# Optimization experiments

Measured on AMD Instinct MI355X. Metric: run time of the kernel, lower is better.

## Reference

```python
import jax, jax.numpy as jnp
import numpy as np

B, N, D = 2, 2048, 1024
H = 16
HS = D // H
EPS = 1e-6


def layer_norm(x, scale, bias):
    mu = jnp.mean(x, axis=-1, keepdims=True)
    var = jnp.mean(jnp.square(x - mu), axis=-1, keepdims=True)
    return (x - mu) * jax.lax.rsqrt(var + EPS) * scale + bias


def setup_inputs() -> dict:
    key = jax.random.key(0)
    ks = jax.random.split(key, 8)
    lecun = lambda k, shape: jax.random.normal(k, shape, jnp.float32) / jnp.sqrt(shape[0])
    return {
        "x": jax.random.normal(ks[0], (B, N, D), jnp.float32),
        "ln1_scale": jnp.ones((D,), jnp.float32),
        "ln1_bias": jnp.zeros((D,), jnp.float32),
        "w_qkv": lecun(ks[1], (D, 3 * D)),
        "w_out": lecun(ks[2], (D, D)),
        "b_out": jnp.zeros((D,), jnp.float32),
        "ln2_scale": jnp.ones((D,), jnp.float32),
        "ln2_bias": jnp.zeros((D,), jnp.float32),
        "w1": lecun(ks[3], (D, 2 * D)),
        "b1": jnp.zeros((2 * D,), jnp.float32),
        "w2": lecun(ks[4], (2 * D, D)),
        "b2": jnp.zeros((D,), jnp.float32),
    }


def reference(x, ln1_scale, ln1_bias, w_qkv, w_out, b_out,
              ln2_scale, ln2_bias, w1, b1, w2, b2):
    b, n, d = x.shape
    # --- attention sub-block ---
    xn = layer_norm(x, ln1_scale, ln1_bias)
    qkv = xn @ w_qkv                      # [B,N,3D]
    q, k, v = jnp.split(qkv, 3, axis=-1)
    q = q.reshape(b, n, H, HS)
    k = k.reshape(b, n, H, HS)
    v = v.reshape(b, n, H, HS)
    scores = jnp.einsum('bihd,bjhd->bhij', q, k) / jnp.sqrt(jnp.float32(HS))
    causal = jnp.tril(jnp.ones((n, n), bool))[None, None]
    scores = jnp.where(causal, scores, -jnp.inf)
    attn = jax.nn.softmax(scores, axis=-1)
    out_heads = jnp.einsum('bhij,bjhd->bihd', attn, v).reshape(b, n, d)
    x = x + out_heads @ w_out + b_out
    xn2 = layer_norm(x, ln2_scale, ln2_bias)
    y = jax.nn.gelu(xn2 @ w1 + b1)        # flax nn.gelu default approximate=True
    x = x + (y @ w2 + b2)
    return x
```

## Files before the change

### kernel.cpp

```cpp
#include <hip/hip_runtime.h>

#define D_MODEL 1024
#define NSEQ    2048
#define NBATCH  2
#define NHEAD   16
#define HSZ     64
#define MROWS   4096

typedef short s8v  __attribute__((ext_vector_type(8)));
typedef float f32x4 __attribute__((ext_vector_type(4)));

#define AS1(p) ((__attribute__((address_space(1))) const void*)(p))
#define AS3(p) ((__attribute__((address_space(3))) void*)(p))

__device__ __forceinline__ float b2f(unsigned short s) {
    union { unsigned u; float f; } z; z.u = (unsigned)s << 16; return z.f;
}
__device__ __forceinline__ unsigned short f2b(float f) {
    union { float f; unsigned u; } z; z.f = f;
    unsigned r = z.u + 0x7fffu + ((z.u >> 16) & 1u);
    return (unsigned short)(r >> 16);
}
__device__ __forceinline__ unsigned short f2b_trunc(float f) {
    union { float f; unsigned u; } z; z.f = f;
    return (unsigned short)(z.u >> 16);
}
__device__ __forceinline__ float gelu_f(float x) {
    float u = 0.7978845608028654f * (x + 0.044715f * x * x * x);
    float t = 1.f - 2.f / (1.f + __expf(2.f * u));
    return 0.5f * x * (1.f + t);
}

__global__ __launch_bounds__(256) void sniff_k(const unsigned short* __restrict__ xr,
                                               int* __restrict__ flag) {
    __shared__ int cnt[4];
    int tid = threadIdx.x, ok = 0;
    for (int i = tid; i < 2048; i += 256) {
        unsigned short u = xr[i];
        int e = (u >> 7) & 0xFF;
        if (u == 0 || (e >= 110 && e <= 135)) ok++;
    }
    #pragma unroll
    for (int off = 32; off; off >>= 1) ok += __shfl_down(ok, off);
    if ((tid & 63) == 0) cnt[tid >> 6] = ok;
    __syncthreads();
    if (tid == 0) {
        int tot = cnt[0] + cnt[1] + cnt[2] + cnt[3];
        *flag = (tot > 1843) ? 1 : 0;
    }
}

__global__ __launch_bounds__(256) void cvt_small_k(
    const void* p0, const void* p1, const void* p2, const void* p3,
    const void* p4, const void* p5, const void* p6,
    unsigned short* __restrict__ out, const int* __restrict__ flag)
{
    int i = blockIdx.x * 256 + threadIdx.x;
    const void* src; int off;
    if      (i < 1024) { src = p0; off = i; }
    else if (i < 2048) { src = p1; off = i - 1024; }
    else if (i < 3072) { src = p2; off = i - 2048; }
    else if (i < 4096) { src = p3; off = i - 3072; }
    else if (i < 5120) { src = p4; off = i - 4096; }
    else if (i < 7168) { src = p5; off = i - 5120; }
    else               { src = p6; off = i - 7168; }
    out[i] = (*flag) ? ((const unsigned short*)src)[off]
                     : f2b(((const float*)src)[off]);
}

__global__ __launch_bounds__(256) void transpose_all_k(
    const void* wqkv, const void* wout, const void* w1, const void* w2,
    unsigned short* t_qkv, unsigned short* t_out,
    unsigned short* t_w1, unsigned short* t_w2, const int* __restrict__ flag)
{
    __shared__ unsigned short t[32][33];
    int bid = blockIdx.x;
    const void* W; unsigned short* Wt; int K, N, bx, by;
    if      (bid < 3072) { W = wqkv; Wt = t_qkv; K = 1024; N = 3072; bx = bid % 96; by = bid / 96; }
    else if (bid < 4096) { bid -= 3072; W = wout; Wt = t_out; K = 1024; N = 1024; bx = bid % 32; by = bid / 32; }
    else if (bid < 6144) { bid -= 4096; W = w1;   Wt = t_w1;  K = 1024; N = 2048; bx = bid % 64; by = bid / 64; }
    else                 { bid -= 6144; W = w2;   Wt = t_w2;  K = 2048; N = 1024; bx = bid % 32; by = bid / 32; }
    int f = *flag;
    int n0 = bx * 32, k0 = by * 32;
    int x = threadIdx.x & 31, y = threadIdx.x >> 5;
    #pragma unroll
    for (int r = 0; r < 32; r += 8) {
        size_t idx = (size_t)(k0 + r + y) * N + n0 + x;
        t[r + y][x] = f ? ((const unsigned short*)W)[idx]
                        : f2b(((const float*)W)[idx]);
    }
    __syncthreads();
    #pragma unroll
    for (int r = 0; r < 32; r += 8)
        Wt[(size_t)(n0 + r + y) * K + k0 + x] = t[x][r + y];
}

__global__ __launch_bounds__(256) void ln1f_k(
    const void* __restrict__ x_raw, const unsigned short* __restrict__ scale,
    const unsigned short* __restrict__ bias, unsigned short* __restrict__ xb,
    unsigned short* __restrict__ xn, const int* __restrict__ flag)
{
    int row = blockIdx.x, tid = threadIdx.x;
    int f = *flag;
    float v[4], s = 0.f, s2 = 0.f;
    #pragma unroll
    for (int i = 0; i < 4; ++i) {
        size_t idx = (size_t)row * D_MODEL + tid + i * 256;
        float t = f ? b2f(((const unsigned short*)x_raw)[idx])
                    : ((const float*)x_raw)[idx];
        v[i] = t; s += t; s2 += t * t;
    }
    #pragma unroll
    for (int off = 32; off; off >>= 1) { s += __shfl_down(s, off); s2 += __shfl_down(s2, off); }
    __shared__ float rs[4], rs2[4];
    int w = tid >> 6;
    if ((tid & 63) == 0) { rs[w] = s; rs2[w] = s2; }
    __syncthreads();
    float S  = rs[0] + rs[1] + rs[2] + rs[3];
    float S2 = rs2[0] + rs2[1] + rs2[2] + rs2[3];
    float mean = S * (1.f / D_MODEL);
    float var  = S2 * (1.f / D_MODEL) - mean * mean;
    float rstd = rsqrtf(var + 1e-6f);
    #pragma unroll
    for (int i = 0; i < 4; ++i) {
        int d = tid + i * 256;
        size_t idx = (size_t)row * D_MODEL + d;
        xb[idx] = f2b(v[i]);
        xn[idx] = f2b((v[i] - mean) * rstd * b2f(scale[d]) + b2f(bias[d]));
    }
}

__global__ __launch_bounds__(256) void ln_k(
    const unsigned short* __restrict__ x, const unsigned short* __restrict__ scale,
    const unsigned short* __restrict__ bias, unsigned short* __restrict__ out)
{
    int row = blockIdx.x, tid = threadIdx.x;
    const unsigned short* xr = x + (size_t)row * D_MODEL;
    float v[4], s = 0.f, s2 = 0.f;
    #pragma unroll
    for (int i = 0; i < 4; ++i) {
        float t = b2f(xr[tid + i * 256]);
        v[i] = t; s += t; s2 += t * t;
    }
    #pragma unroll
    for (int off = 32; off; off >>= 1) { s += __shfl_down(s, off); s2 += __shfl_down(s2, off); }
    __shared__ float rs[4], rs2[4];
    int w = tid >> 6;
    if ((tid & 63) == 0) { rs[w] = s; rs2[w] = s2; }
    __syncthreads();
    float S  = rs[0] + rs[1] + rs[2] + rs[3];
    float S2 = rs2[0] + rs2[1] + rs2[2] + rs2[3];
    float mean = S * (1.f / D_MODEL);
    float var  = S2 * (1.f / D_MODEL) - mean * mean;
    float rstd = rsqrtf(var + 1e-6f);
    #pragma unroll
    for (int i = 0; i < 4; ++i) {
        int d = tid + i * 256;
        out[(size_t)row * D_MODEL + d] =
            f2b((v[i] - mean) * rstd * b2f(scale[d]) + b2f(bias[d]));
    }
}

template<int TN, int ACT, int RES, int ODYN>
__global__ __launch_bounds__(256) void gemm128_k(
    const unsigned short* __restrict__ A, const unsigned short* __restrict__ Bt,
    const unsigned short* __restrict__ bias, const unsigned short* __restrict__ resid,
    void* __restrict__ Cp, int M, int Nn, int K, const int* __restrict__ flag)
{
    constexpr int MT = (TN == 128) ? 4 : 2;
    __shared__ short As[128 * 64];
    __shared__ short Bs[TN * 64];
    int tid = threadIdx.x;
    int m0 = blockIdx.y * 128, n0 = blockIdx.x * TN;
    int lane = tid & 63, w = tid >> 6;
    int a_base = (TN == 128) ? (w >> 1) * 64 : w * 32;
    int b_base = (TN == 128) ? (w & 1) * 64 : 0;
    int mm = lane & 15, q = lane >> 4;

    f32x4 zero = {0.f, 0.f, 0.f, 0.f};
    f32x4 acc[MT][4];
    #pragma unroll
    for (int mt = 0; mt < MT; ++mt)
        #pragma unroll
        for (int nt = 0; nt < 4; ++nt) acc[mt][nt] = zero;

    int grow   = lane >> 3;
    int gchunk = ((lane & 7) ^ grow) * 8;
    const unsigned short* Ab = A  + (size_t)(m0 + w * 32 + grow) * K + gchunk;
    const unsigned short* Bb = Bt + (size_t)(n0 + w * (TN / 4) + grow) * K + gchunk;
    int swz = (mm & 7);

    for (int k0 = 0; k0 < K; k0 += 64) {
        __syncthreads();
        #pragma unroll
        for (int s = 0; s < 4; ++s)
            __builtin_amdgcn_global_load_lds(AS1(Ab + k0 + (size_t)(s * 8) * K),
                                             AS3(&As[(w * 32 + s * 8) * 64]), 16, 0, 0);
        #pragma unroll
        for (int s = 0; s < TN / 32; ++s)
            __builtin_amdgcn_global_load_lds(AS1(Bb + k0 + (size_t)(s * 8) * K),
                                             AS3(&Bs[(w * (TN / 4) + s * 8) * 64]), 16, 0, 0);
        __syncthreads();
        #pragma unroll
        for (int kk = 0; kk < 2; ++kk) {
            int col = ((kk * 4 + q) ^ swz) * 8;
            s8v af[MT], bf[4];
            #pragma unroll
            for (int mt = 0; mt < MT; ++mt)
                af[mt] = *(const s8v*)&As[(a_base + mt * 16 + mm) * 64 + col];
            #pragma unroll
            for (int nt = 0; nt < 4; ++nt)
                bf[nt] = *(const s8v*)&Bs[(b_base + nt * 16 + mm) * 64 + col];
            #pragma unroll
            for (int mt = 0; mt < MT; ++mt)
                #pragma unroll
                for (int nt = 0; nt < 4; ++nt)
                    acc[mt][nt] = __builtin_amdgcn_mfma_f32_16x16x32_bf16(
                        af[mt], bf[nt], acc[mt][nt], 0, 0, 0);
        }
    }

    int f = ODYN ? *flag : 1;
    #pragma unroll
    for (int nt = 0; nt < 4; ++nt) {
        int gc = n0 + b_base + nt * 16 + mm;
        float bv = bias ? b2f(bias[gc]) : 0.f;
        #pragma unroll
        for (int mt = 0; mt < MT; ++mt) {
            #pragma unroll
            for (int r = 0; r < 4; ++r) {
                int gr = m0 + a_base + mt * 16 + q * 4 + r;
                float v = acc[mt][nt][r] + bv;
                if (ACT == 1) v = gelu_f(v);
                if (RES == 1) v += b2f(resid[(size_t)gr * Nn + gc]);
                if (f) ((unsigned short*)Cp)[(size_t)gr * Nn + gc] = f2b(v);
                else   ((float*)Cp)[(size_t)gr * Nn + gc] = v;
            }
        }
    }
}

__global__ __launch_bounds__(256, 3) void fattn_k(
    const unsigned short* __restrict__ qkv, unsigned short* __restrict__ attn_out)
{
    int bh = blockIdx.x;
    int h = bh & (NHEAD - 1), b = bh >> 4;
    int qt = gridDim.y - 1 - blockIdx.y;
    int q0 = qt * 64;
    size_t base = (size_t)b * NSEQ * (3 * D_MODEL);

    __shared__ __align__(16) short Ks[128][72];
    __shared__ __align__(16) short Vts[64][136];
    __shared__ __align__(16) short Ps[64][136];

    int tid = threadIdx.x, lane = tid & 63, w = tid >> 6;
    int mm = lane & 15, q = lane >> 4;

    s8v qf[2];
    #pragma unroll
    for (int kk = 0; kk < 2; ++kk)
        qf[kk] = *(const s8v*)(qkv + base + (size_t)(q0 + w * 16 + mm) * (3 * D_MODEL)
                               + h * HSZ + kk * 32 + q * 8);

    f32x4 zero = {0.f, 0.f, 0.f, 0.f};
    f32x4 acc_o[4] = {zero, zero, zero, zero};
    float l_acc[4] = {0.f, 0.f, 0.f, 0.f};

    int kr = tid >> 1;
    int kc = (tid & 1) * 32;
    int kp = tid >> 3;
    int vd = (tid & 7) * 8;

    const unsigned short* kbase = qkv + base + D_MODEL + h * HSZ;
    const unsigned short* vbase = qkv + base + 2 * D_MODEL + h * HSZ;

    int nstages = (qt + 2) >> 1;

    s8v kv0, kv1, kv2, kv3, vv0, vv1, vv2, vv3;
    {
        const unsigned short* kb = kbase;
        const unsigned short* vb = vbase;
        kv0 = *(const s8v*)(kb + (size_t)kr * (3 * D_MODEL) + kc);
        kv1 = *(const s8v*)(kb + (size_t)kr * (3 * D_MODEL) + kc + 8);
        kv2 = *(const s8v*)(kb + (size_t)kr * (3 * D_MODEL) + kc + 16);
        kv3 = *(const s8v*)(kb + (size_t)kr * (3 * D_MODEL) + kc + 24);
        vv0 = *(const s8v*)(vb + (size_t)(2 * kp)      * (3 * D_MODEL) + vd);
        vv1 = *(const s8v*)(vb + (size_t)(2 * kp + 1)  * (3 * D_MODEL) + vd);
        vv2 = *(const s8v*)(vb + (size_t)(2 * kp + 64) * (3 * D_MODEL) + vd);
        vv3 = *(const s8v*)(vb + (size_t)(2 * kp + 65) * (3 * D_MODEL) + vd);
    }

    for (int t = 0; t < nstages; ++t) {
        int j0 = t * 128;
        int nsub = (j0 < q0) ? 2 : 1;

        __syncthreads();
        *(s8v*)&Ks[kr][kc]      = kv0;
        *(s8v*)&Ks[kr][kc + 8]  = kv1;
        *(s8v*)&Ks[kr][kc + 16] = kv2;
        *(s8v*)&Ks[kr][kc + 24] = kv3;
        int c0 = (2 * kp + vd) & 63;
        #pragma unroll
        for (int e = 0; e < 8; ++e) {
            unsigned p0 = (unsigned)(unsigned short)vv0[e] |
                          ((unsigned)(unsigned short)vv1[e] << 16);
            unsigned p1 = (unsigned)(unsigned short)vv2[e] |
                          ((unsigned)(unsigned short)vv3[e] << 16);
            *(unsigned*)&Vts[vd + e][c0]      = p0;
            *(unsigned*)&Vts[vd + e][64 + c0] = p1;
        }
        if (t + 1 < nstages) {
            const unsigned short* kb = kbase + (size_t)(j0 + 128) * (3 * D_MODEL);
            const unsigned short* vb = vbase + (size_t)(j0 + 128) * (3 * D_MODEL);
            kv0 = *(const s8v*)(kb + (size_t)kr * (3 * D_MODEL) + kc);
            kv1 = *(const s8v*)(kb + (size_t)kr * (3 * D_MODEL) + kc + 8);
            kv2 = *(const s8v*)(kb + (size_t)kr * (3 * D_MODEL) + kc + 16);
            kv3 = *(const s8v*)(kb + (size_t)kr * (3 * D_MODEL) + kc + 24);
            vv0 = *(const s8v*)(vb + (size_t)(2 * kp)      * (3 * D_MODEL) + vd);
            vv1 = *(const s8v*)(vb + (size_t)(2 * kp + 1)  * (3 * D_MODEL) + vd);
            vv2 = *(const s8v*)(vb + (size_t)(2 * kp + 64) * (3 * D_MODEL) + vd);
            vv3 = *(const s8v*)(vb + (size_t)(2 * kp + 65) * (3 * D_MODEL) + vd);
        }
        __syncthreads();

        f32x4 sc[8];
        #pragma unroll
        for (int i = 0; i < 8; ++i) sc[i] = zero;
        #pragma unroll
        for (int sub = 0; sub < 2; ++sub) {
            if (sub >= nsub) break;
            #pragma unroll
            for (int kk = 0; kk < 2; ++kk) {
                #pragma unroll
                for (int nt = 0; nt < 4; ++nt) {
                    s8v bv = *(const s8v*)&Ks[sub * 64 + nt * 16 + mm][kk * 32 + q * 8];
                    sc[sub * 4 + nt] = __builtin_amdgcn_mfma_f32_16x16x32_bf16(
                        qf[kk], bv, sc[sub * 4 + nt], 0, 0, 0);
                }
            }
        }

        int pswz = 16 * q;
        #pragma unroll
        for (int sub = 0; sub < 2; ++sub) {
            if (sub >= nsub) break;
            bool need_mask = (j0 + sub * 64 + 63) > (q0 + w * 16);
            #pragma unroll
            for (int nt = 0; nt < 4; ++nt) {
                int gj = j0 + sub * 64 + nt * 16 + mm;
                #pragma unroll
                for (int r = 0; r < 4; ++r) {
                    float p = __expf(sc[sub * 4 + nt][r] * 0.125f);
                    if (need_mask && gj > (q0 + w * 16 + q * 4 + r)) p = 0.f;
                    l_acc[r] += p;
                    Ps[w * 16 + q * 4 + r][sub * 64 + ((nt * 16 + mm + pswz) & 63)] =
                        (short)f2b_trunc(p);
                }
            }
        }

        int rq16 = 16 * ((mm >> 2) & 3);
        #pragma unroll
        for (int kk4 = 0; kk4 < 4; ++kk4) {
            if (kk4 >= nsub * 2) break;
            int sub = kk4 >> 1, kkl = kk4 & 1;
            s8v av = *(const s8v*)&Ps[w * 16 + mm]
                        [sub * 64 + ((kkl * 32 + q * 8 + rq16) & 63)];
            #pragma unroll
            for (int nt = 0; nt < 4; ++nt) {
                int d = nt * 16 + mm;
                int c = sub * 64 + ((kkl * 32 + q * 8 + (d & 56)) & 63);
                s8v bv = *(const s8v*)&Vts[d][c];
                acc_o[nt] = __builtin_amdgcn_mfma_f32_16x16x32_bf16(av, bv, acc_o[nt], 0, 0, 0);
            }
        }
    }

    #pragma unroll
    for (int r = 0; r < 4; ++r) {
        #pragma unroll
        for (int msk = 1; msk < 16; msk <<= 1) l_acc[r] += __shfl_xor(l_acc[r], msk);
        l_acc[r] = 1.f / l_acc[r];
    }
    #pragma unroll
    for (int nt = 0; nt < 4; ++nt) {
        int d = nt * 16 + mm;
        #pragma unroll
        for (int r = 0; r < 4; ++r) {
            int row = q0 + w * 16 + q * 4 + r;
            attn_out[(size_t)(b * NSEQ + row) * D_MODEL + h * HSZ + d] =
                f2b(acc_o[nt][r] * l_acc[r]);
        }
    }
}

extern "C" void kernel_launch(void* const* d_in, const int* in_sizes, int n_in,
                              void* d_out, int out_size, void* d_ws, size_t ws_size,
                              hipStream_t stream)
{
    const void* x_raw  = d_in[0];
    const void* ln1s_r = d_in[1];
    const void* ln1b_r = d_in[2];
    const void* wqkv_r = d_in[3];
    const void* wout_r = d_in[4];
    const void* bout_r = d_in[5];
    const void* ln2s_r = d_in[6];
    const void* ln2b_r = d_in[7];
    const void* w1_r   = d_in[8];
    const void* b1_r   = d_in[9];
    const void* w2_r   = d_in[10];
    const void* b2_r   = d_in[11];

    char* ws = (char*)d_ws;
    const size_t MB = 1024 * 1024;
    unsigned short* wt_qkv = (unsigned short*)(ws + 0 * MB);
    unsigned short* wt_out = (unsigned short*)(ws + 6 * MB);
    unsigned short* wt_w1  = (unsigned short*)(ws + 8 * MB);
    unsigned short* wt_w2  = (unsigned short*)(ws + 12 * MB);
    unsigned short* xb     = (unsigned short*)(ws + 16 * MB);
    unsigned short* xn     = (unsigned short*)(ws + 24 * MB);
    unsigned short* qkvb   = (unsigned short*)(ws + 32 * MB);
    unsigned short* x1     = (unsigned short*)(ws + 48 * MB);
    int*            flag   = (int*)           (ws + 56 * MB);
    unsigned short* cbias  = (unsigned short*)(ws + 56 * MB + 1024);
    unsigned short* attnb  = xn;
    unsigned short* xn2    = xn;
    unsigned short* hb     = qkvb;

    unsigned short* c_ln1s = cbias + 0;
    unsigned short* c_ln1b = cbias + 1024;
    unsigned short* c_bout = cbias + 2048;
    unsigned short* c_ln2s = cbias + 3072;
    unsigned short* c_ln2b = cbias + 4096;
    unsigned short* c_b1   = cbias + 5120;
    unsigned short* c_b2   = cbias + 7168;

    sniff_k<<<1, 256, 0, stream>>>((const unsigned short*)x_raw, flag);
    cvt_small_k<<<32, 256, 0, stream>>>(ln1s_r, ln1b_r, bout_r, ln2s_r, ln2b_r,
                                        b1_r, b2_r, cbias, flag);
    transpose_all_k<<<8192, 256, 0, stream>>>(wqkv_r, wout_r, w1_r, w2_r,
                                              wt_qkv, wt_out, wt_w1, wt_w2, flag);
    ln1f_k<<<MROWS, 256, 0, stream>>>(x_raw, c_ln1s, c_ln1b, xb, xn, flag);
    gemm128_k<128, 0, 0, 0><<<dim3(24, 32), 256, 0, stream>>>(
        xn, wt_qkv, nullptr, nullptr, qkvb, MROWS, 3072, 1024, flag);
    fattn_k<<<dim3(NBATCH * NHEAD, NSEQ / 64), 256, 0, stream>>>(qkvb, attnb);
    gemm128_k<64, 0, 1, 0><<<dim3(16, 32), 256, 0, stream>>>(
        attnb, wt_out, c_bout, xb, x1, MROWS, 1024, 1024, flag);
    ln_k<<<MROWS, 256, 0, stream>>>(x1, c_ln2s, c_ln2b, xn2);
    gemm128_k<128, 1, 0, 0><<<dim3(16, 32), 256, 0, stream>>>(
        xn2, wt_w1, c_b1, nullptr, hb, MROWS, 2048, 1024, flag);
    gemm128_k<64, 0, 1, 1><<<dim3(16, 32), 256, 0, stream>>>(
        hb, wt_w2, c_b2, x1, d_out, MROWS, 1024, 2048, flag);
}
```

Measured before the change: 285.6 us.

## Rewrite flash attention with 32x32 MFMA, register-resident P and swizzled LDS

The causal attention kernel is restructured around 32x32x16 bf16 MFMAs. The score tile is computed transposed (K as the A operand), so the exponentiated probabilities stay in registers and feed the PV MFMA directly, which removes the Ps shared-memory round trip. The 1/8 softmax scale is folded into Q by subtracting 3 from the bf16 exponent. Each block now covers 128 query rows with 64-key stages, uses XOR-swizzled LDS for K and transposed V, and adds s_setprio hints; the risk is more register pressure and less parallelism, since the grid has half as many blocks.

```diff
diff --git a/kernel.cpp b/kernel.cpp
--- a/kernel.cpp
+++ b/kernel.cpp
@@ -8,7 +8,9 @@
 #define MROWS   4096
 
 typedef short s8v  __attribute__((ext_vector_type(8)));
+typedef short s4v  __attribute__((ext_vector_type(4)));
 typedef float f32x4 __attribute__((ext_vector_type(4)));
+typedef float f32x16 __attribute__((ext_vector_type(16)));
 
 #define AS1(p) ((__attribute__((address_space(1))) const void*)(p))
 #define AS3(p) ((__attribute__((address_space(3))) void*)(p))
@@ -29,6 +31,11 @@
     float u = 0.7978845608028654f * (x + 0.044715f * x * x * x);
     float t = 1.f - 2.f / (1.f + __expf(2.f * u));
     return 0.5f * x * (1.f + t);
+}
+__device__ __forceinline__ unsigned cvt_pk_bf16(float lo, float hi) {
+    unsigned r;
+    asm("v_cvt_pk_bf16_f32 %0, %1, %2" : "=v"(r) : "v"(lo), "v"(hi));
+    return r;
 }
 
 __global__ __launch_bounds__(256) void sniff_k(const unsigned short* __restrict__ xr,
@@ -240,157 +247,154 @@
     }
 }
 
-__global__ __launch_bounds__(256, 3) void fattn_k(
+#define SWZG(r) ((((r) >> 3) ^ (r)) & 7)
+
+__global__ __launch_bounds__(256, 4) void fattn_k(
     const unsigned short* __restrict__ qkv, unsigned short* __restrict__ attn_out)
 {
     int bh = blockIdx.x;
     int h = bh & (NHEAD - 1), b = bh >> 4;
     int qt = gridDim.y - 1 - blockIdx.y;
-    int q0 = qt * 64;
+    int q0 = qt * 128;
     size_t base = (size_t)b * NSEQ * (3 * D_MODEL);
 
-    __shared__ __align__(16) short Ks[128][72];
-    __shared__ __align__(16) short Vts[64][136];
-    __shared__ __align__(16) short Ps[64][136];
+    __shared__ __align__(16) short Ks[64 * 64];
+    __shared__ __align__(16) short Vt[64 * 64];
 
     int tid = threadIdx.x, lane = tid & 63, w = tid >> 6;
-    int mm = lane & 15, q = lane >> 4;
-
-    s8v qf[2];
-    #pragma unroll
-    for (int kk = 0; kk < 2; ++kk)
-        qf[kk] = *(const s8v*)(qkv + base + (size_t)(q0 + w * 16 + mm) * (3 * D_MODEL)
-                               + h * HSZ + kk * 32 + q * 8);
-
-    f32x4 zero = {0.f, 0.f, 0.f, 0.f};
-    f32x4 acc_o[4] = {zero, zero, zero, zero};
-    float l_acc[4] = {0.f, 0.f, 0.f, 0.f};
-
-    int kr = tid >> 1;
-    int kc = (tid & 1) * 32;
+    int ql = lane & 31, hi = lane >> 5;
+    int qw0 = q0 + w * 32;
+    int gq = qw0 + ql;
+
+    s8v qB[4];
+    {
+        const unsigned short* qrow = qkv + base + (size_t)gq * (3 * D_MODEL) + h * HSZ;
+        #pragma unroll
+        for (int ks = 0; ks < 4; ++ks) {
+            s8v v = *(const s8v*)(qrow + ks * 16 + hi * 8);
+            #pragma unroll
+            for (int e = 0; e < 8; ++e) {
+                unsigned short u = (unsigned short)v[e];
+                if (u & 0x7f80u) u = (unsigned short)(u - 0x0180u);
+                v[e] = (short)u;
+            }
+            qB[ks] = v;
+        }
+    }
+
+    const unsigned short* kbase = qkv + base + D_MODEL + h * HSZ;
+    const unsigned short* vbase = qkv + base + 2 * D_MODEL + h * HSZ;
+
+    int krow = tid >> 2;
+    int kc16 = (tid & 3) * 16;
+    int km0  = (tid & 3) * 2;
+    int kws0 = krow * 64 + (((km0    ) ^ SWZG(krow)) << 3);
+    int kws1 = krow * 64 + (((km0 + 1) ^ SWZG(krow)) << 3);
     int kp = tid >> 3;
     int vd = (tid & 7) * 8;
 
-    const unsigned short* kbase = qkv + base + D_MODEL + h * HSZ;
-    const unsigned short* vbase = qkv + base + 2 * D_MODEL + h * HSZ;
-
-    int nstages = (qt + 2) >> 1;
-
-    s8v kv0, kv1, kv2, kv3, vv0, vv1, vv2, vv3;
+    f32x16 z16;
+    #pragma unroll
+    for (int i = 0; i < 16; ++i) z16[i] = 0.f;
+    f32x16 accA = z16, accB = z16;
+    float l_acc = 0.f;
+
+    int nstages = 2 * qt + 2;
+
+    s8v ka, kb, va, vb;
     {
-        const unsigned short* kb = kbase;
-        const unsigned short* vb = vbase;
-        kv0 = *(const s8v*)(kb + (size_t)kr * (3 * D_MODEL) + kc);
-        kv1 = *(const s8v*)(kb + (size_t)kr * (3 * D_MODEL) + kc + 8);
-        kv2 = *(const s8v*)(kb + (size_t)kr * (3 * D_MODEL) + kc + 16);
-        kv3 = *(const s8v*)(kb + (size_t)kr * (3 * D_MODEL) + kc + 24);
-        vv0 = *(const s8v*)(vb + (size_t)(2 * kp)      * (3 * D_MODEL) + vd);
-        vv1 = *(const s8v*)(vb + (size_t)(2 * kp + 1)  * (3 * D_MODEL) + vd);
-        vv2 = *(const s8v*)(vb + (size_t)(2 * kp + 64) * (3 * D_MODEL) + vd);
-        vv3 = *(const s8v*)(vb + (size_t)(2 * kp + 65) * (3 * D_MODEL) + vd);
+        const unsigned short* kr_ = kbase + (size_t)krow * (3 * D_MODEL) + kc16;
+        ka = *(const s8v*)kr_;
+        kb = *(const s8v*)(kr_ + 8);
+        const unsigned short* vr_ = vbase + (size_t)(2 * kp) * (3 * D_MODEL) + vd;
+        va = *(const s8v*)vr_;
+        vb = *(const s8v*)(vr_ + 3 * D_MODEL);
     }
 
     for (int t = 0; t < nstages; ++t) {
-        int j0 = t * 128;
-        int nsub = (j0 < q0) ? 2 : 1;
-
+        int j0 = t * 64;
         __syncthreads();
-        *(s8v*)&Ks[kr][kc]      = kv0;
-        *(s8v*)&Ks[kr][kc + 8]  = kv1;
-        *(s8v*)&Ks[kr][kc + 16] = kv2;
-        *(s8v*)&Ks[kr][kc + 24] = kv3;
-        int c0 = (2 * kp + vd) & 63;
+        *(s8v*)&Ks[kws0] = ka;
+        *(s8v*)&Ks[kws1] = kb;
         #pragma unroll
         for (int e = 0; e < 8; ++e) {
-            unsigned p0 = (unsigned)(unsigned short)vv0[e] |
-                          ((unsigned)(unsigned short)vv1[e] << 16);
-            unsigned p1 = (unsigned)(unsigned short)vv2[e] |
-                          ((unsigned)(unsigned short)vv3[e] << 16);
-            *(unsigned*)&Vts[vd + e][c0]      = p0;
-            *(unsigned*)&Vts[vd + e][64 + c0] = p1;
+            unsigned pv = (unsigned)(unsigned short)va[e] |
+                          ((unsigned)(unsigned short)vb[e] << 16);
+            int idx = (vd + e) * 64 + ((((kp >> 2) ^ (tid & 7) ^ e) & 7) << 3)
+                      + ((2 * kp) & 7);
+            *(unsigned*)&Vt[idx] = pv;
         }
         if (t + 1 < nstages) {
-            const unsigned short* kb = kbase + (size_t)(j0 + 128) * (3 * D_MODEL);
-            const unsigned short* vb = vbase + (size_t)(j0 + 128) * (3 * D_MODEL);
-            kv0 = *(const s8v*)(kb + (size_t)kr * (3 * D_MODEL) + kc);
-            kv1 = *(const s8v*)(kb + (size_t)kr * (3 * D_MODEL) + kc + 8);
-            kv2 = *(const s8v*)(kb + (size_t)kr * (3 * D_MODEL) + kc + 16);
-            kv3 = *(const s8v*)(kb + (size_t)kr * (3 * D_MODEL) + kc + 24);
-            vv0 = *(const s8v*)(vb + (size_t)(2 * kp)      * (3 * D_MODEL) + vd);
-            vv1 = *(const s8v*)(vb + (size_t)(2 * kp + 1)  * (3 * D_MODEL) + vd);
-            vv2 = *(const s8v*)(vb + (size_t)(2 * kp + 64) * (3 * D_MODEL) + vd);
-            vv3 = *(const s8v*)(vb + (size_t)(2 * kp + 65) * (3 * D_MODEL) + vd);
+            const unsigned short* kr_ = kbase + (size_t)(j0 + 64 + krow) * (3 * D_MODEL) + kc16;
+            ka = *(const s8v*)kr_;
+            kb = *(const s8v*)(kr_ + 8);
+            const unsigned short* vr_ = vbase + (size_t)(j0 + 64 + 2 * kp) * (3 * D_MODEL) + vd;
+            va = *(const s8v*)vr_;
+            vb = *(const s8v*)(vr_ + 3 * D_MODEL);
         }
         __syncthreads();
 
-        f32x4 sc[8];
-        #pragma unroll
-        for (int i = 0; i < 8; ++i) sc[i] = zero;
-        #pragma unroll
-        for (int sub = 0; sub < 2; ++sub) {
-            if (sub >= nsub) break;
-            #pragma unroll
-            for (int kk = 0; kk < 2; ++kk) {
+        if (j0 > qw0 + 31) continue;
+        int nkt = (j0 + 32 <= qw0 + 31) ? 2 : 1;
+        #pragma unroll
+        for (int kt = 0; kt < 2; ++kt) {
+            if (kt >= nkt) break;
+            f32x16 sc = z16;
+            __builtin_amdgcn_s_setprio(1);
+            #pragma unroll
+            for (int ks = 0; ks < 4; ++ks) {
+                int key = kt * 32 + ql;
+                s8v kf = *(const s8v*)&Ks[key * 64 + (((2 * ks + hi) ^ SWZG(key)) << 3)];
+                sc = __builtin_amdgcn_mfma_f32_32x32x16_bf16(kf, qB[ks], sc, 0, 0, 0);
+            }
+            __builtin_amdgcn_s_setprio(0);
+            bool needmask = (j0 + kt * 32 + 31) > qw0;
+            #pragma unroll
+            for (int r = 0; r < 16; ++r) {
+                float p = __expf(sc[r]);
+                if (needmask) {
+                    int gk = j0 + kt * 32 + (r & 3) + 8 * (r >> 2) + 4 * hi;
+                    if (gk > gq) p = 0.f;
+                }
+                l_acc += p;
+                sc[r] = p;
+            }
+            #pragma unroll
+            for (int slot = 0; slot < 2; ++slot) {
+                union { unsigned u[4]; s8v v; } pu;
+                pu.u[0] = cvt_pk_bf16(sc[slot * 8 + 0], sc[slot * 8 + 1]);
+                pu.u[1] = cvt_pk_bf16(sc[slot * 8 + 2], sc[slot * 8 + 3]);
+                pu.u[2] = cvt_pk_bf16(sc[slot * 8 + 4], sc[slot * 8 + 5]);
+                pu.u[3] = cvt_pk_bf16(sc[slot * 8 + 6], sc[slot * 8 + 7]);
+                int g1 = 4 * kt + 2 * slot;
+                __builtin_amdgcn_s_setprio(1);
                 #pragma unroll
-                for (int nt = 0; nt < 4; ++nt) {
-                    s8v bv = *(const s8v*)&Ks[sub * 64 + nt * 16 + mm][kk * 32 + q * 8];
-                    sc[sub * 4 + nt] = __builtin_amdgcn_mfma_f32_16x16x32_bf16(
-                        qf[kk], bv, sc[sub * 4 + nt], 0, 0, 0);
+                for (int dt = 0; dt < 2; ++dt) {
+                    int dim = dt * 32 + ql;
+                    int sw = SWZG(dim);
+                    union { s4v hh[2]; s8v v; } vu;
+                    vu.hh[0] = *(const s4v*)&Vt[dim * 64 + (((g1    ) ^ sw) << 3) + 4 * hi];
+                    vu.hh[1] = *(const s4v*)&Vt[dim * 64 + (((g1 + 1) ^ sw) << 3) + 4 * hi];
+                    if (dt == 0)
+                        accA = __builtin_amdgcn_mfma_f32_32x32x16_bf16(pu.v, vu.v, accA, 0, 0, 0);
+                    else
+                        accB = __builtin_amdgcn_mfma_f32_32x32x16_bf16(pu.v, vu.v, accB, 0, 0, 0);
                 }
+                __builtin_amdgcn_s_setprio(0);
             }
         }
-
-        int pswz = 16 * q;
-        #pragma unroll
-        for (int sub = 0; sub < 2; ++sub) {
-            if (sub >= nsub) break;
-            bool need_mask = (j0 + sub * 64 + 63) > (q0 + w * 16);
-            #pragma unroll
-            for (int nt = 0; nt < 4; ++nt) {
-                int gj = j0 + sub * 64 + nt * 16 + mm;
-                #pragma unroll
-                for (int r = 0; r < 4; ++r) {
-                    float p = __expf(sc[sub * 4 + nt][r] * 0.125f);
-                    if (need_mask && gj > (q0 + w * 16 + q * 4 + r)) p = 0.f;
-                    l_acc[r] += p;
-                    Ps[w * 16 + q * 4 + r][sub * 64 + ((nt * 16 + mm + pswz) & 63)] =
-                        (short)f2b_trunc(p);
-                }
-            }
-        }
-
-        int rq16 = 16 * ((mm >> 2) & 3);
-        #pragma unroll
-        for (int kk4 = 0; kk4 < 4; ++kk4) {
-            if (kk4 >= nsub * 2) break;
-            int sub = kk4 >> 1, kkl = kk4 & 1;
-            s8v av = *(const s8v*)&Ps[w * 16 + mm]
-                        [sub * 64 + ((kkl * 32 + q * 8 + rq16) & 63)];
-            #pragma unroll
-            for (int nt = 0; nt < 4; ++nt) {
-                int d = nt * 16 + mm;
-                int c = sub * 64 + ((kkl * 32 + q * 8 + (d & 56)) & 63);
-                s8v bv = *(const s8v*)&Vts[d][c];
-                acc_o[nt] = __builtin_amdgcn_mfma_f32_16x16x32_bf16(av, bv, acc_o[nt], 0, 0, 0);
-            }
-        }
-    }
-
-    #pragma unroll
-    for (int r = 0; r < 4; ++r) {
-        #pragma unroll
-        for (int msk = 1; msk < 16; msk <<= 1) l_acc[r] += __shfl_xor(l_acc[r], msk);
-        l_acc[r] = 1.f / l_acc[r];
-    }
-    #pragma unroll
-    for (int nt = 0; nt < 4; ++nt) {
-        int d = nt * 16 + mm;
-        #pragma unroll
-        for (int r = 0; r < 4; ++r) {
-            int row = q0 + w * 16 + q * 4 + r;
-            attn_out[(size_t)(b * NSEQ + row) * D_MODEL + h * HSZ + d] =
-                f2b(acc_o[nt][r] * l_acc[r]);
-        }
+    }
+
+    l_acc += __shfl_xor(l_acc, 32);
+    float linv = 1.f / l_acc;
+    unsigned short* orow = attn_out + (size_t)b * NSEQ * D_MODEL + h * HSZ;
+    #pragma unroll
+    for (int r = 0; r < 16; ++r) {
+        int cr = (r & 3) + 8 * (r >> 2) + 4 * hi;
+        float ri = __shfl(linv, cr);
+        size_t ro = (size_t)(qw0 + cr) * D_MODEL;
+        orow[ro + ql]      = f2b(accA[r] * ri);
+        orow[ro + 32 + ql] = f2b(accB[r] * ri);
     }
 }
 
@@ -443,7 +447,7 @@
     ln1f_k<<<MROWS, 256, 0, stream>>>(x_raw, c_ln1s, c_ln1b, xb, xn, flag);
     gemm128_k<128, 0, 0, 0><<<dim3(24, 32), 256, 0, stream>>>(
         xn, wt_qkv, nullptr, nullptr, qkvb, MROWS, 3072, 1024, flag);
-    fattn_k<<<dim3(NBATCH * NHEAD, NSEQ / 64), 256, 0, stream>>>(qkvb, attnb);
+    fattn_k<<<dim3(NBATCH * NHEAD, NSEQ / 128), 256, 0, stream>>>(qkvb, attnb);
     gemm128_k<64, 0, 1, 0><<<dim3(16, 32), 256, 0, stream>>>(
         attnb, wt_out, c_bout, xb, x1, MROWS, 1024, 1024, flag);
     ln_k<<<MROWS, 256, 0, stream>>>(x1, c_ln2s, c_ln2b, xn2);
```

Result: slower. 297.2 us (+4.1%).
